# Performance work log

Hardware: AMD Instinct MI355X
Metric: run time of the kernel (lower is better)

The kernel has to match this reference:

```python
import jax, jax.numpy as jnp
import numpy as np

B, F, V = 64, 256, 128   # groups, frames/group, vecs/group (uniform ragged groups)
CF = 512                 # cross_feature


def setup_inputs() -> dict:
    key = jax.random.key(0)
    ks = jax.random.split(key, 18)
    p = lambda k, s: jax.random.normal(k, s, jnp.float32) * 0.02
    return {
        "metas": jax.random.uniform(ks[0], (B, 5), jnp.float32),
        "meta_indexs": jnp.arange(B),
        "frames": jax.random.normal(ks[1], (B * F, 600), jnp.float32),
        "frame_indexs": jnp.repeat(jnp.arange(B), F),
        "vecs": jax.random.normal(ks[2], (B * V, 768), jnp.float32),
        "vec_indexs": jnp.repeat(jnp.arange(B), V),
        "audios": jax.random.normal(ks[3], (B, 128), jnp.float32),
        "audio_indexs": jnp.arange(B),
        "Wfk": p(ks[4], (CF, 600)), "Wfv": p(ks[5], (CF, 600)),
        "Wvk": p(ks[6], (CF, 768)), "Wvv": p(ks[7], (CF, 768)),
        "Wav": p(ks[8], (CF, 128)),
        "Wff_f": p(ks[9], (2, CF, CF)),
        "Wff_v": p(ks[10], (2, CF, CF)),
        "Wff_a": p(ks[11], (2, CF, CF)),
        "Wout1": p(ks[12], (768, 3 * CF + 3)),
        "Wout2": p(ks[13], (512, 768)),
        "Wout3": p(ks[14], (64, 512)),
        "Wout4": p(ks[15], (1, 64)),
    }


def reference(metas, meta_indexs, frames, frame_indexs, vecs, vec_indexs,
              audios, audio_indexs, Wfk, Wfv, Wvk, Wvv, Wav,
              Wff_f, Wff_v, Wff_a, Wout1, Wout2, Wout3, Wout4):
    # groups are uniform: reshape ragged rows into [B, n, d] (indexes are
    # contiguous repeats per setup_inputs, so the mask-gathers become reshapes)
    b = audios.shape[0]
    fb = frames.reshape(b, -1, frames.shape[-1])   # [B,F,600]
    vb = vecs.reshape(b, -1, vecs.shape[-1])       # [B,V,768]
    relu = jax.nn.relu

    f_k = relu(jnp.einsum('bfd,cd->bfc', fb, Wfk))     # [B,F,CF]
    f_v = relu(jnp.einsum('bfd,cd->bfc', fb, Wfv))
    v_k = relu(jnp.einsum('bvd,cd->bvc', vb, Wvk))     # [B,V,CF]
    v_v = relu(jnp.einsum('bvd,cd->bvc', vb, Wvv))
    a_v = relu(audios @ Wav.T)                         # [B,CF]

    # torch: softmax(mm(k, q)) with no dim on an (N,1) tensor -> dim=1 -> ones,
    # so the initial "attended" queries are plain sums of the value projections.
    f_q_p = f_v.sum(axis=1)                            # [B,CF]
    v_q_p = v_v.sum(axis=1)
    a_q_p = a_v                                        # single audio row

    for i in range(2):
        attn_f = jax.nn.softmax(jnp.einsum('bfc,bc->bf', f_k, v_q_p) / CF, axis=1)
        f_c = jnp.einsum('bf,bfc->bc', attn_f, f_v)
        f_q_n = f_c @ Wff_f[i].T + f_q_p
        attn_v = jax.nn.softmax(jnp.einsum('bvc,bc->bv', v_k, v_q_p) / CF, axis=1)
        v_c = jnp.einsum('bv,bvc->bc', attn_v, v_v)
        v_q_n = v_c @ Wff_v[i].T + v_q_p
        # audio attention is softmax over a single element -> weight 1
        a_q_n = a_v @ Wff_a[i].T + a_q_p
        f_q_p, v_q_p, a_q_p = f_q_n, v_q_n, a_q_n      # dropout is dead code

    mean = a_q_p.mean(axis=1, keepdims=True)
    std = a_q_p.std(axis=1, keepdims=True, ddof=1)     # torch.std is unbiased
    na = (a_q_p - mean) / std

    goal = metas[:, 1:2] / 1500.0
    dura = metas[:, 3:4] - metas[:, 2:3]
    dura = jnp.where(dura > 8000.0, 100.0, dura) / 100.0
    create = metas[:, 4:5] / 5.0

    feats = jnp.concatenate([f_q_p, v_q_p, na, goal, create, dura], axis=1)  # [B,1539]
    h = relu(feats @ Wout1.T)
    h = relu(h @ Wout2.T)
    h = relu(h @ Wout3.T)
    out = jax.nn.sigmoid(h @ Wout4.T)                  # [B,1]
    return out[:, 0]
```

## Files before the change

### kernel.cpp

```cpp
#include <hip/hip_runtime.h>
#include <hip/hip_bf16.h>

typedef __attribute__((ext_vector_type(4))) float f32x4;
typedef __attribute__((ext_vector_type(8))) __bf16 bf16x8;
typedef __attribute__((ext_vector_type(8))) unsigned short us8;
typedef __attribute__((ext_vector_type(4))) unsigned int u32x4;

#define LDS_AS __attribute__((address_space(3)))
#define GLB_AS __attribute__((address_space(1)))

__device__ __forceinline__ float bf2f(unsigned short h) {
    return __builtin_bit_cast(float, (unsigned)h << 16);
}
__device__ __forceinline__ unsigned short f2bf(float f) {
    return __builtin_bit_cast(unsigned short, (__bf16)f);
}
__device__ __forceinline__ us8 cvt8(f32x4 a, f32x4 b) {
    bf16x8 r;
    r[0] = (__bf16)a[0]; r[1] = (__bf16)a[1]; r[2] = (__bf16)a[2]; r[3] = (__bf16)a[3];
    r[4] = (__bf16)b[0]; r[5] = (__bf16)b[1]; r[6] = (__bf16)b[2]; r[7] = (__bf16)b[3];
    return __builtin_bit_cast(us8, r);
}
__device__ __forceinline__ void cp16(const void* g, void* l) {
    __builtin_amdgcn_global_load_lds((const GLB_AS unsigned int*)g,
                                     (LDS_AS unsigned int*)l, 16, 0, 0);
}

#define NPREPB 2048
#define NTOT 2588672
__global__ __launch_bounds__(256) void prep_kernel(
    const float* __restrict__ frames, const float* __restrict__ Wfk, const float* __restrict__ Wfv,
    const float* __restrict__ vecs, const float* __restrict__ Wvk, const float* __restrict__ Wvv,
    const float* __restrict__ Wout1, const float* __restrict__ audios, const float* __restrict__ Wav,
    unsigned short* __restrict__ fbf, unsigned short* __restrict__ wf,
    unsigned short* __restrict__ vbf, unsigned short* __restrict__ wv,
    float* __restrict__ W1p, float* __restrict__ hacc, float* __restrict__ qz,
    float* __restrict__ a_v, float* __restrict__ a_q_p)
{
    __shared__ float aud[128];
    const int t = threadIdx.x;
    if (blockIdx.x >= NPREPB) {
        const int b = blockIdx.x - NPREPB;
        if (t < 128) aud[t] = audios[b * 128 + t];
        __syncthreads();
        #pragma unroll
        for (int cc = 0; cc < 2; ++cc) {
            int c = 2 * t + cc;
            const float* wr = Wav + (size_t)c * 128;
            float s = 0.f;
            #pragma unroll
            for (int k4 = 0; k4 < 32; ++k4) {
                f32x4 wvv = *(const f32x4*)(wr + k4 * 4);
                s += wvv[0] * aud[k4 * 4] + wvv[1] * aud[k4 * 4 + 1]
                   + wvv[2] * aud[k4 * 4 + 2] + wvv[3] * aud[k4 * 4 + 3];
            }
            s = s > 0.f ? s : 0.f;
            a_v[b * 512 + c] = s;
            a_q_p[b * 512 + c] = s;
        }
        return;
    }
    for (int i = blockIdx.x * 256 + t; i < NTOT; i += NPREPB * 256) {
        int idx = i;
        if (idx < 1245184) {
            int row = idx / 76, k = (idx - row * 76) * 8;
            us8 o = {0, 0, 0, 0, 0, 0, 0, 0};
            if (k < 600) {
                const float* s = frames + (size_t)row * 600 + k;
                o = cvt8(*(const f32x4*)s, *(const f32x4*)(s + 4));
            }
            *(us8*)(fbf + (size_t)row * 608 + k) = o;
            continue;
        }
        idx -= 1245184;
        if (idx < 77824) {
            int row = idx / 76, k = (idx - row * 76) * 8;
            const float* src = row < 512 ? Wfk + (size_t)row * 600 : Wfv + (size_t)(row - 512) * 600;
            us8 o = {0, 0, 0, 0, 0, 0, 0, 0};
            if (k < 600) o = cvt8(*(const f32x4*)(src + k), *(const f32x4*)(src + k + 4));
            *(us8*)(wf + (size_t)row * 608 + k) = o;
            continue;
        }
        idx -= 77824;
        if (idx < 786432) {
            int row = idx / 96, k = (idx - row * 96) * 8;
            const float* s = vecs + (size_t)row * 768 + k;
            *(us8*)(vbf + (size_t)row * 768 + k) = cvt8(*(const f32x4*)s, *(const f32x4*)(s + 4));
            continue;
        }
        idx -= 786432;
        if (idx < 98304) {
            int row = idx / 96, k = (idx - row * 96) * 8;
            const float* src = (row < 512 ? Wvk + (size_t)row * 768
                                          : Wvv + (size_t)(row - 512) * 768) + k;
            *(us8*)(wv + (size_t)row * 768 + k) = cvt8(*(const f32x4*)src, *(const f32x4*)(src + 4));
            continue;
        }
        idx -= 98304;
        if (idx < 344064) {
            int r = idx / 448, k = (idx - r * 448) * 4;
            f32x4 o;
            #pragma unroll
            for (int j = 0; j < 4; ++j) {
                int kk = k + j;
                o[j] = kk < 1539 ? Wout1[(size_t)r * 1539 + kk] : 0.f;
            }
            *(f32x4*)(W1p + (size_t)r * 1792 + k) = o;
            continue;
        }
        idx -= 344064;
        if (idx < 20480) {
            f32x4 z = {0, 0, 0, 0};
            *(f32x4*)(hacc + (size_t)idx * 4) = z;
            continue;
        }
        idx -= 20480;
        {
            f32x4 z = {0, 0, 0, 0};
            *(f32x4*)(qz + (size_t)idx * 4) = z;
        }
    }
}

__global__ __launch_bounds__(256) void gemm_bt_relu(
    const unsigned short* __restrict__ Af, const unsigned short* __restrict__ Bf,
    unsigned short* __restrict__ Cfo, float* __restrict__ qf,
    const unsigned short* __restrict__ Av, const unsigned short* __restrict__ Bv,
    unsigned short* __restrict__ Cvo, float* __restrict__ qv)
{
    __shared__ alignas(16) unsigned short sA[3][4096];
    __shared__ alignas(16) unsigned short sB[3][4096];
    const int t = threadIdx.x;
    const int w = t >> 6, l = t & 63;
    const unsigned short *A, *B;
    unsigned short* C;
    float* qout;
    int Kp, ktiles, gshift, nwg, pb;
    if (blockIdx.x < 1024) { A = Af; B = Bf; C = Cfo; qout = qf; Kp = 608; ktiles = 19; gshift = 8; nwg = 1024; pb = blockIdx.x; }
    else                   { A = Av; B = Bv; C = Cvo; qout = qv; Kp = 768; ktiles = 24; gshift = 7; nwg = 512;  pb = blockIdx.x - 1024; }
    const int swz = (pb & 7) * (nwg >> 3) + (pb >> 3);
    const int bm = swz >> 3, bn = swz & 7;
    const int m0 = bm << 7, n0 = bn << 7;

    const int srow = t >> 2, sk0 = (t & 3) << 3;
    const unsigned short* gA = A + (size_t)(m0 + srow) * Kp + sk0;
    const unsigned short* gB = B + (size_t)(n0 + srow) * Kp + sk0;

    const int wr = w >> 1, wc = w & 1;
    const int fAoff = (wr * 64 + (l & 15)) * 32 + ((l >> 4) << 3);
    const int fBoff = (wc * 64 + (l & 15)) * 32 + ((l >> 4) << 3);

    auto stage = [&](int buf, int kt) {
        char* lA = (char*)(&sA[buf][0]) + w * 1024;
        char* lB = (char*)(&sB[buf][0]) + w * 1024;
        const unsigned short* ga = gA + kt * 32;
        const unsigned short* gb = gB + kt * 32;
        cp16(ga, lA);
        cp16(ga + (size_t)64 * Kp, lA + 4096);
        cp16(gb, lB);
        cp16(gb + (size_t)64 * Kp, lB + 4096);
    };

    stage(0, 0);
    stage(1, 1);
    f32x4 acc[4][4] = {};
    int cur = 0;
    for (int kt = 0; kt < ktiles; ++kt) {
        if (kt + 1 < ktiles) {
            asm volatile("s_waitcnt vmcnt(4)" ::: "memory");
        } else {
            asm volatile("s_waitcnt vmcnt(0)" ::: "memory");
        }
        __builtin_amdgcn_sched_barrier(0);
        __builtin_amdgcn_s_barrier();
        __builtin_amdgcn_sched_barrier(0);

        bf16x8 af[4], bfr[4];
        #pragma unroll
        for (int i = 0; i < 4; ++i) {
            af[i]  = *(const bf16x8*)(&sA[cur][0] + fAoff + i * 512);
            bfr[i] = *(const bf16x8*)(&sB[cur][0] + fBoff + i * 512);
        }
        #pragma unroll
        for (int mi = 0; mi < 4; ++mi)
            #pragma unroll
            for (int ni = 0; ni < 4; ++ni)
                acc[mi][ni] = __builtin_amdgcn_mfma_f32_16x16x32_bf16(af[mi], bfr[ni], acc[mi][ni], 0, 0, 0);

        if (kt + 2 < ktiles) {
            int b2 = cur + 2; if (b2 >= 3) b2 -= 3;
            stage(b2, kt + 2);
        }
        cur = (cur + 1 == 3) ? 0 : cur + 1;
    }

    const int crow0 = m0 + wr * 64 + ((l >> 4) << 2);
    const int ccol0 = n0 + wc * 64 + (l & 15);
    #pragma unroll
    for (int mi = 0; mi < 4; ++mi)
        #pragma unroll
        for (int ni = 0; ni < 4; ++ni)
            #pragma unroll
            for (int j = 0; j < 4; ++j) {
                float v = acc[mi][ni][j];
                v = v > 0.f ? v : 0.f;
                C[(size_t)(crow0 + mi * 16 + j) * 1024 + (ccol0 + ni * 16)] = f2bf(v);
            }
    if (n0 >= 512) {
        const int g = m0 >> gshift;
        float csum[4];
        #pragma unroll
        for (int ni = 0; ni < 4; ++ni) {
            float s = 0.f;
            #pragma unroll
            for (int mi = 0; mi < 4; ++mi)
                #pragma unroll
                for (int j = 0; j < 4; ++j)
                    s += fmaxf(acc[mi][ni][j], 0.f);
            s += __shfl_xor(s, 16, 64);
            s += __shfl_xor(s, 32, 64);
            csum[ni] = s;
        }
        if (l < 16) {
            #pragma unroll
            for (int ni = 0; ni < 4; ++ni)
                atomicAdd(&qout[g * 512 + (ccol0 - 512) + ni * 16], csum[ni]);
        }
    }
}

__global__ __launch_bounds__(256) void scores_kernel(
    const unsigned short* __restrict__ Cf, const unsigned short* __restrict__ Cv,
    const float* __restrict__ v_q_p, float* __restrict__ sbuf, float* __restrict__ fvz)
{
    const int t = threadIdx.x, bid = blockIdx.x;
    if (bid < 64) {
        f32x4 z = {0, 0, 0, 0};
        ((f32x4*)fvz)[bid * 256 + t] = z;
    }
    const int w = t >> 6, l = t & 63;
    int fbase, g, soff;
    const unsigned short* X;
    if (bid < 1024) { fbase = bid * 16 + w * 4; g = fbase >> 8; X = Cf; soff = 0; }
    else            { fbase = (bid - 1024) * 16 + w * 4; g = fbase >> 7; X = Cv; soff = 16384; }
    const float* vq = v_q_p + g * 512 + l * 8;
    f32x4 q0 = *(const f32x4*)vq;
    f32x4 q1 = *(const f32x4*)(vq + 4);
    #pragma unroll
    for (int i = 0; i < 4; ++i) {
        const int frame = fbase + i;
        u32x4 u = *(const u32x4*)(X + (size_t)frame * 1024 + l * 8);
        float acc = q0[0] * bf2f((unsigned short)(u[0] & 0xffff)) + q0[1] * bf2f((unsigned short)(u[0] >> 16))
                  + q0[2] * bf2f((unsigned short)(u[1] & 0xffff)) + q0[3] * bf2f((unsigned short)(u[1] >> 16))
                  + q1[0] * bf2f((unsigned short)(u[2] & 0xffff)) + q1[1] * bf2f((unsigned short)(u[2] >> 16))
                  + q1[2] * bf2f((unsigned short)(u[3] & 0xffff)) + q1[3] * bf2f((unsigned short)(u[3] >> 16));
        #pragma unroll
        for (int m = 1; m < 64; m <<= 1) acc += __shfl_xor(acc, m, 64);
        if (l == 0) sbuf[soff + frame] = acc * (1.f / 512.f);
    }
}

__global__ __launch_bounds__(256) void pv_kernel(
    const unsigned short* __restrict__ Cf, const unsigned short* __restrict__ Cv,
    const float* __restrict__ sbuf, float* __restrict__ fc, float* __restrict__ vc)
{
    __shared__ float ws[256];
    __shared__ float red[256];
    const int t = threadIdx.x, bid = blockIdx.x;
    int g, chunk, NF, soff;
    const unsigned short* X;
    float* outp;
    if (bid < 1024) { g = bid >> 4; chunk = bid & 15; NF = 256; X = Cf; soff = g * 256; outp = fc; }
    else { int b2 = bid - 1024; g = b2 >> 3; chunk = b2 & 7; NF = 128; X = Cv; soff = 16384 + g * 128; outp = vc; }
    float s = (t < NF) ? sbuf[soff + t] : -1e30f;
    red[t] = s;
    __syncthreads();
    for (int st = 128; st > 0; st >>= 1) { if (t < st) red[t] = fmaxf(red[t], red[t + st]); __syncthreads(); }
    float m = red[0];
    __syncthreads();
    float e = (t < NF) ? __expf(s - m) : 0.f;
    ws[t] = e;
    red[t] = e;
    __syncthreads();
    for (int st = 128; st > 0; st >>= 1) { if (t < st) red[t] += red[t + st]; __syncthreads(); }
    float inv = 1.f / red[0];
    const int f0 = g * NF + chunk * 16;
    const unsigned int* q = (const unsigned int*)X + (size_t)f0 * 512 + 256 + t;
    float s0 = 0.f, s1 = 0.f;
    #pragma unroll 4
    for (int f = 0; f < 16; ++f) {
        float a = ws[chunk * 16 + f];
        unsigned u = q[(size_t)f * 512];
        s0 += a * bf2f((unsigned short)(u & 0xffff));
        s1 += a * bf2f((unsigned short)(u >> 16));
    }
    atomicAdd(&outp[g * 512 + 2 * t],     s0 * inv);
    atomicAdd(&outp[g * 512 + 2 * t + 1], s1 * inv);
}

__device__ __forceinline__ void gemv_body(
    const float* __restrict__ X, int ldx, int dorelu,
    const float* __restrict__ W, int ldw, float* __restrict__ Y, int ldy,
    int nc, int kc, int bc)
{
    __shared__ float xs[4096];
    const int t = threadIdx.x;
    #pragma unroll
    for (int j = 0; j < 16; ++j) {
        int idx = t + j * 256;
        float v = X[(size_t)(bc * 32 + (idx >> 7)) * ldx + kc * 128 + (idx & 127)];
        xs[idx] = dorelu ? (v > 0.f ? v : 0.f) : v;
    }
    __syncthreads();
    const int r = t & 63, bg = t >> 6;
    const int row = nc * 64 + r;
    const float* wrow = W + (size_t)row * ldw + kc * 128;
    float acc[8] = {};
    #pragma unroll 8
    for (int k4 = 0; k4 < 32; ++k4) {
        f32x4 wvv = *(const f32x4*)(wrow + k4 * 4);
        #pragma unroll
        for (int bb = 0; bb < 8; ++bb) {
            f32x4 xv = *(const f32x4*)(xs + (bg * 8 + bb) * 128 + k4 * 4);
            acc[bb] += wvv[0] * xv[0] + wvv[1] * xv[1] + wvv[2] * xv[2] + wvv[3] * xv[3];
        }
    }
    #pragma unroll
    for (int bb = 0; bb < 8; ++bb)
        atomicAdd(&Y[(size_t)(bc * 32 + bg * 8 + bb) * ldy + row], acc[bb]);
}

__global__ __launch_bounds__(256) void update_kernel(
    const float* __restrict__ Wff_f, const float* __restrict__ Wff_v, const float* __restrict__ Wff_a,
    int iter, const float* __restrict__ fc, const float* __restrict__ vc, const float* __restrict__ a_v,
    float* __restrict__ f_q_p, float* __restrict__ v_q_p, float* __restrict__ a_q_p)
{
    int id = blockIdx.x;
    const int op = id >> 6; id &= 63;
    const int nc = id & 7, kc = (id >> 3) & 3, bc = id >> 5;
    const float* W = (op == 0 ? Wff_f : op == 1 ? Wff_v : Wff_a) + (size_t)iter * 262144;
    const float* X = op == 0 ? fc : op == 1 ? vc : a_v;
    float* Y = op == 0 ? f_q_p : op == 1 ? v_q_p : a_q_p;
    gemv_body(X, 512, 0, W, 512, Y, 512, nc, kc, bc);
}

__global__ __launch_bounds__(256) void gemvb_kernel(
    const float* __restrict__ X, int ldx, int dorelu,
    const float* __restrict__ W, int ldw, float* __restrict__ Y, int ldy,
    int NC, int KC)
{
    int bid = blockIdx.x;
    const int nc = bid % NC; bid /= NC;
    const int kc = bid % KC;
    const int bc = bid / KC;
    gemv_body(X, ldx, dorelu, W, ldw, Y, ldy, nc, kc, bc);
}

__global__ __launch_bounds__(512) void normfeats_kernel(
    const float* __restrict__ a_q_p, const float* __restrict__ f_q_p, const float* __restrict__ v_q_p,
    const float* __restrict__ metas, float* __restrict__ feats)
{
    __shared__ float red[512];
    const int t = threadIdx.x, b = blockIdx.x;
    float a = a_q_p[b * 512 + t];
    red[t] = a;
    __syncthreads();
    for (int s = 256; s > 0; s >>= 1) { if (t < s) red[t] += red[t + s]; __syncthreads(); }
    float mean = red[0] * (1.f / 512.f);
    __syncthreads();
    float d = a - mean;
    red[t] = d * d;
    __syncthreads();
    for (int s = 256; s > 0; s >>= 1) { if (t < s) red[t] += red[t + s]; __syncthreads(); }
    float sd = sqrtf(red[0] * (1.f / 511.f));
    float* fr = feats + (size_t)b * 1792;
    fr[t]        = f_q_p[b * 512 + t];
    fr[512 + t]  = v_q_p[b * 512 + t];
    fr[1024 + t] = d / sd;
    if (t < 256) {
        float v = 0.f;
        if (t == 0) v = metas[b * 5 + 1] * (1.f / 1500.f);
        else if (t == 1) v = metas[b * 5 + 4] * 0.2f;
        else if (t == 2) {
            float du = metas[b * 5 + 3] - metas[b * 5 + 2];
            v = (du > 8000.f ? 100.f : du) * 0.01f;
        }
        fr[1536 + t] = v;
    }
}

__global__ __launch_bounds__(256) void mlp34_kernel(
    const float* __restrict__ h2acc, const float* __restrict__ W3, const float* __restrict__ W4,
    float* __restrict__ out)
{
    __shared__ float xs[512];
    __shared__ float part[256];
    __shared__ float h3[64];
    const int t = threadIdx.x, b = blockIdx.x;
    {
        float v0 = h2acc[(size_t)b * 512 + t];
        float v1 = h2acc[(size_t)b * 512 + 256 + t];
        xs[t] = v0 > 0.f ? v0 : 0.f;
        xs[256 + t] = v1 > 0.f ? v1 : 0.f;
    }
    __syncthreads();
    const int r = t & 63, q = t >> 6;
    const float* wrow = W3 + (size_t)r * 512 + q * 128;
    float acc = 0.f;
    #pragma unroll 8
    for (int k4 = 0; k4 < 32; ++k4) {
        f32x4 wvv = *(const f32x4*)(wrow + k4 * 4);
        f32x4 xv  = *(const f32x4*)(xs + q * 128 + k4 * 4);
        acc += wvv[0] * xv[0] + wvv[1] * xv[1] + wvv[2] * xv[2] + wvv[3] * xv[3];
    }
    part[t] = acc;
    __syncthreads();
    if (t < 64) {
        float h = part[t] + part[t + 64] + part[t + 128] + part[t + 192];
        h3[t] = h > 0.f ? h : 0.f;
    }
    __syncthreads();
    if (t < 64) {
        float v = h3[t] * W4[t];
        #pragma unroll
        for (int m = 1; m < 64; m <<= 1) v += __shfl_xor(v, m, 64);
        if (t == 0) out[b] = 1.f / (1.f + __expf(-v));
    }
}

extern "C" void kernel_launch(void* const* d_in, const int* in_sizes, int n_in,
                              void* d_out, int out_size, void* d_ws, size_t ws_size,
                              hipStream_t stream)
{
    const float* metas  = (const float*)d_in[0];
    const float* frames = (const float*)d_in[2];
    const float* vecs   = (const float*)d_in[4];
    const float* audios = (const float*)d_in[6];
    const float* Wfk   = (const float*)d_in[8];
    const float* Wfv   = (const float*)d_in[9];
    const float* Wvk   = (const float*)d_in[10];
    const float* Wvv   = (const float*)d_in[11];
    const float* Wav   = (const float*)d_in[12];
    const float* Wff_f = (const float*)d_in[13];
    const float* Wff_v = (const float*)d_in[14];
    const float* Wff_a = (const float*)d_in[15];
    const float* Wout1 = (const float*)d_in[16];
    const float* Wout2 = (const float*)d_in[17];
    const float* Wout3 = (const float*)d_in[18];
    const float* Wout4 = (const float*)d_in[19];
    float* out = (float*)d_out;

    char* p = (char*)d_ws;
    auto alloc = [&](size_t n) { char* r = p; p += (n + 255) & ~(size_t)255; return r; };
    unsigned short* fbf = (unsigned short*)alloc(16384ull * 608 * 2);
    unsigned short* wf  = (unsigned short*)alloc(1024ull * 608 * 2);
    unsigned short* vbf = (unsigned short*)alloc(8192ull * 768 * 2);
    unsigned short* wv  = (unsigned short*)alloc(1024ull * 768 * 2);
    unsigned short* Cf  = (unsigned short*)alloc(16384ull * 1024 * 2);
    unsigned short* Cv  = (unsigned short*)alloc(8192ull * 1024 * 2);
    float* W1p   = (float*)alloc(768ull * 1792 * 4);
    float* feats = (float*)alloc(64ull * 1792 * 4);
    float* qbuf  = (float*)alloc(2ull * 64 * 512 * 4);
    float* f_q_p = qbuf;
    float* v_q_p = qbuf + 64 * 512;
    float* a_q_p = (float*)alloc(64ull * 512 * 4);
    float* a_v   = (float*)alloc(64ull * 512 * 4);
    float* fvc   = (float*)alloc(2ull * 64 * 512 * 4);
    float* fcb   = fvc;
    float* vcb   = fvc + 64 * 512;
    float* hacc  = (float*)alloc(81920ull * 4);
    float* h1acc = hacc;
    float* h2acc = hacc + 64 * 768;
    float* sbuf  = (float*)alloc(24576ull * 4);

    prep_kernel<<<NPREPB + 64, 256, 0, stream>>>(frames, Wfk, Wfv, vecs, Wvk, Wvv, Wout1,
                                                 audios, Wav, fbf, wf, vbf, wv, W1p, hacc,
                                                 qbuf, a_v, a_q_p);
    gemm_bt_relu<<<1536, 256, 0, stream>>>(fbf, wf, Cf, f_q_p, vbf, wv, Cv, v_q_p);
    for (int i = 0; i < 2; ++i) {
        scores_kernel<<<1536, 256, 0, stream>>>(Cf, Cv, v_q_p, sbuf, fvc);
        pv_kernel<<<1536, 256, 0, stream>>>(Cf, Cv, sbuf, fcb, vcb);
        update_kernel<<<192, 256, 0, stream>>>(Wff_f, Wff_v, Wff_a, i, fcb, vcb, a_v,
                                               f_q_p, v_q_p, a_q_p);
    }
    normfeats_kernel<<<64, 512, 0, stream>>>(a_q_p, f_q_p, v_q_p, metas, feats);
    gemvb_kernel<<<336, 256, 0, stream>>>(feats, 1792, 0, W1p, 1792, h1acc, 768, 12, 14);
    gemvb_kernel<<<96, 256, 0, stream>>>(h1acc, 768, 1, Wout2, 768, h2acc, 512, 8, 6);
    mlp34_kernel<<<64, 256, 0, stream>>>(h2acc, Wout3, Wout4, out);
}
```

Measured before the change: 176.4 us.

## Fuse fp32-to-bf16 activation conversion into the projection GEMM A-tile load

```diff
diff --git a/kernel.cpp b/kernel.cpp
--- a/kernel.cpp
+++ b/kernel.cpp
@@ -3,6 +3,7 @@
 
 typedef __attribute__((ext_vector_type(4))) float f32x4;
 typedef __attribute__((ext_vector_type(8))) __bf16 bf16x8;
+typedef __attribute__((ext_vector_type(4))) unsigned short us4;
 typedef __attribute__((ext_vector_type(8))) unsigned short us8;
 typedef __attribute__((ext_vector_type(4))) unsigned int u32x4;
 
@@ -26,14 +27,13 @@
                                      (LDS_AS unsigned int*)l, 16, 0, 0);
 }
 
-#define NPREPB 2048
-#define NTOT 2588672
+#define NPREPB 544
+#define NTOT 557056
 __global__ __launch_bounds__(256) void prep_kernel(
-    const float* __restrict__ frames, const float* __restrict__ Wfk, const float* __restrict__ Wfv,
-    const float* __restrict__ vecs, const float* __restrict__ Wvk, const float* __restrict__ Wvv,
+    const float* __restrict__ Wfk, const float* __restrict__ Wfv,
+    const float* __restrict__ Wvk, const float* __restrict__ Wvv,
     const float* __restrict__ Wout1, const float* __restrict__ audios, const float* __restrict__ Wav,
-    unsigned short* __restrict__ fbf, unsigned short* __restrict__ wf,
-    unsigned short* __restrict__ vbf, unsigned short* __restrict__ wv,
+    unsigned short* __restrict__ wf, unsigned short* __restrict__ wv,
     float* __restrict__ W1p, float* __restrict__ hacc, float* __restrict__ qz,
     float* __restrict__ a_v, float* __restrict__ a_q_p)
 {
@@ -62,17 +62,6 @@
     }
     for (int i = blockIdx.x * 256 + t; i < NTOT; i += NPREPB * 256) {
         int idx = i;
-        if (idx < 1245184) {
-            int row = idx / 76, k = (idx - row * 76) * 8;
-            us8 o = {0, 0, 0, 0, 0, 0, 0, 0};
-            if (k < 600) {
-                const float* s = frames + (size_t)row * 600 + k;
-                o = cvt8(*(const f32x4*)s, *(const f32x4*)(s + 4));
-            }
-            *(us8*)(fbf + (size_t)row * 608 + k) = o;
-            continue;
-        }
-        idx -= 1245184;
         if (idx < 77824) {
             int row = idx / 76, k = (idx - row * 76) * 8;
             const float* src = row < 512 ? Wfk + (size_t)row * 600 : Wfv + (size_t)(row - 512) * 600;
@@ -82,13 +71,6 @@
             continue;
         }
         idx -= 77824;
-        if (idx < 786432) {
-            int row = idx / 96, k = (idx - row * 96) * 8;
-            const float* s = vecs + (size_t)row * 768 + k;
-            *(us8*)(vbf + (size_t)row * 768 + k) = cvt8(*(const f32x4*)s, *(const f32x4*)(s + 4));
-            continue;
-        }
-        idx -= 786432;
         if (idx < 98304) {
             int row = idx / 96, k = (idx - row * 96) * 8;
             const float* src = (row < 512 ? Wvk + (size_t)row * 768
@@ -122,58 +104,78 @@
     }
 }
 
-__global__ __launch_bounds__(256) void gemm_bt_relu(
-    const unsigned short* __restrict__ Af, const unsigned short* __restrict__ Bf,
+__global__ __launch_bounds__(256) void gemm_fused(
+    const float* __restrict__ Aff, const unsigned short* __restrict__ Bf,
     unsigned short* __restrict__ Cfo, float* __restrict__ qf,
-    const unsigned short* __restrict__ Av, const unsigned short* __restrict__ Bv,
+    const float* __restrict__ Afv, const unsigned short* __restrict__ Bv,
     unsigned short* __restrict__ Cvo, float* __restrict__ qv)
 {
     __shared__ alignas(16) unsigned short sA[3][4096];
     __shared__ alignas(16) unsigned short sB[3][4096];
     const int t = threadIdx.x;
     const int w = t >> 6, l = t & 63;
-    const unsigned short *A, *B;
+    const float* A;
+    const unsigned short* B;
     unsigned short* C;
     float* qout;
-    int Kp, ktiles, gshift, nwg, pb;
-    if (blockIdx.x < 1024) { A = Af; B = Bf; C = Cfo; qout = qf; Kp = 608; ktiles = 19; gshift = 8; nwg = 1024; pb = blockIdx.x; }
-    else                   { A = Av; B = Bv; C = Cvo; qout = qv; Kp = 768; ktiles = 24; gshift = 7; nwg = 512;  pb = blockIdx.x - 1024; }
+    int Kreal, Kp, ktiles, gshift, nwg, pb;
+    if (blockIdx.x < 1024) { A = Aff; B = Bf; C = Cfo; qout = qf; Kreal = 600; Kp = 608; ktiles = 19; gshift = 8; nwg = 1024; pb = blockIdx.x; }
+    else                   { A = Afv; B = Bv; C = Cvo; qout = qv; Kreal = 768; Kp = 768; ktiles = 24; gshift = 7; nwg = 512;  pb = blockIdx.x - 1024; }
     const int swz = (pb & 7) * (nwg >> 3) + (pb >> 3);
     const int bm = swz >> 3, bn = swz & 7;
     const int m0 = bm << 7, n0 = bn << 7;
 
     const int srow = t >> 2, sk0 = (t & 3) << 3;
-    const unsigned short* gA = A + (size_t)(m0 + srow) * Kp + sk0;
     const unsigned short* gB = B + (size_t)(n0 + srow) * Kp + sk0;
+    const int arow = w * 32 + (l >> 3);
+    const int acol = (l & 7) * 4;
+    const float* gA = A + (size_t)(m0 + arow) * Kreal + acol;
+    const int wAidx = arow * 32 + acol;
 
     const int wr = w >> 1, wc = w & 1;
     const int fAoff = (wr * 64 + (l & 15)) * 32 + ((l >> 4) << 3);
     const int fBoff = (wc * 64 + (l & 15)) * 32 + ((l >> 4) << 3);
 
-    auto stage = [&](int buf, int kt) {
-        char* lA = (char*)(&sA[buf][0]) + w * 1024;
+    f32x4 av[4];
+    auto loadA = [&](int kt) {
+        const bool ok = (kt * 32 + acol) < Kreal;
+        const float* ga = gA + kt * 32;
+        #pragma unroll
+        for (int j = 0; j < 4; ++j)
+            av[j] = ok ? *(const f32x4*)(ga + (size_t)j * 8 * Kreal)
+                       : f32x4{0.f, 0.f, 0.f, 0.f};
+    };
+    auto writeA = [&](int buf) {
+        unsigned short* wA = &sA[buf][0] + wAidx;
+        #pragma unroll
+        for (int j = 0; j < 4; ++j) {
+            us4 o = {f2bf(av[j][0]), f2bf(av[j][1]), f2bf(av[j][2]), f2bf(av[j][3])};
+            *(us4*)(wA + j * 256) = o;
+        }
+    };
+    auto stageB = [&](int buf, int kt) {
         char* lB = (char*)(&sB[buf][0]) + w * 1024;
-        const unsigned short* ga = gA + kt * 32;
         const unsigned short* gb = gB + kt * 32;
-        cp16(ga, lA);
-        cp16(ga + (size_t)64 * Kp, lA + 4096);
         cp16(gb, lB);
         cp16(gb + (size_t)64 * Kp, lB + 4096);
     };
 
-    stage(0, 0);
-    stage(1, 1);
+    loadA(0);
+    stageB(0, 0);
+    stageB(1, 1);
+    asm volatile("s_waitcnt vmcnt(4)" ::: "memory");
+    writeA(0);
+    asm volatile("s_waitcnt vmcnt(2)" ::: "memory");
+    asm volatile("s_waitcnt lgkmcnt(0)" ::: "memory");
+    __builtin_amdgcn_s_barrier();
+
     f32x4 acc[4][4] = {};
     int cur = 0;
     for (int kt = 0; kt < ktiles; ++kt) {
-        if (kt + 1 < ktiles) {
-            asm volatile("s_waitcnt vmcnt(4)" ::: "memory");
-        } else {
-            asm volatile("s_waitcnt vmcnt(0)" ::: "memory");
-        }
-        __builtin_amdgcn_sched_barrier(0);
-        __builtin_amdgcn_s_barrier();
-        __builtin_amdgcn_sched_barrier(0);
+        int nxt = cur + 1; if (nxt == 3) nxt = 0;
+        int nx2 = nxt + 1; if (nx2 == 3) nx2 = 0;
+        if (kt + 1 < ktiles) loadA(kt + 1);
+        if (kt + 2 < ktiles) stageB(nx2, kt + 2);
 
         bf16x8 af[4], bfr[4];
         #pragma unroll
@@ -187,11 +189,17 @@
             for (int ni = 0; ni < 4; ++ni)
                 acc[mi][ni] = __builtin_amdgcn_mfma_f32_16x16x32_bf16(af[mi], bfr[ni], acc[mi][ni], 0, 0, 0);
 
-        if (kt + 2 < ktiles) {
-            int b2 = cur + 2; if (b2 >= 3) b2 -= 3;
-            stage(b2, kt + 2);
-        }
-        cur = (cur + 1 == 3) ? 0 : cur + 1;
+        if (kt + 1 < ktiles) {
+            if (kt + 2 < ktiles) asm volatile("s_waitcnt vmcnt(2)" ::: "memory");
+            else                 asm volatile("s_waitcnt vmcnt(0)" ::: "memory");
+            __builtin_amdgcn_sched_barrier(0);
+            writeA(nxt);
+            asm volatile("s_waitcnt lgkmcnt(0)" ::: "memory");
+            __builtin_amdgcn_sched_barrier(0);
+            __builtin_amdgcn_s_barrier();
+            __builtin_amdgcn_sched_barrier(0);
+        }
+        cur = nxt;
     }
 
     const int crow0 = m0 + wr * 64 + ((l >> 4) << 2);
@@ -452,9 +460,7 @@
 
     char* p = (char*)d_ws;
     auto alloc = [&](size_t n) { char* r = p; p += (n + 255) & ~(size_t)255; return r; };
-    unsigned short* fbf = (unsigned short*)alloc(16384ull * 608 * 2);
     unsigned short* wf  = (unsigned short*)alloc(1024ull * 608 * 2);
-    unsigned short* vbf = (unsigned short*)alloc(8192ull * 768 * 2);
     unsigned short* wv  = (unsigned short*)alloc(1024ull * 768 * 2);
     unsigned short* Cf  = (unsigned short*)alloc(16384ull * 1024 * 2);
     unsigned short* Cv  = (unsigned short*)alloc(8192ull * 1024 * 2);
@@ -473,10 +479,9 @@
     float* h2acc = hacc + 64 * 768;
     float* sbuf  = (float*)alloc(24576ull * 4);
 
-    prep_kernel<<<NPREPB + 64, 256, 0, stream>>>(frames, Wfk, Wfv, vecs, Wvk, Wvv, Wout1,
-                                                 audios, Wav, fbf, wf, vbf, wv, W1p, hacc,
-                                                 qbuf, a_v, a_q_p);
-    gemm_bt_relu<<<1536, 256, 0, stream>>>(fbf, wf, Cf, f_q_p, vbf, wv, Cv, v_q_p);
+    prep_kernel<<<NPREPB + 64, 256, 0, stream>>>(Wfk, Wfv, Wvk, Wvv, Wout1, audios, Wav,
+                                                 wf, wv, W1p, hacc, qbuf, a_v, a_q_p);
+    gemm_fused<<<1536, 256, 0, stream>>>(frames, wf, Cf, f_q_p, vecs, wv, Cv, v_q_p);
     for (int i = 0; i < 2; ++i) {
         scores_kernel<<<1536, 256, 0, stream>>>(Cf, Cv, v_q_p, sbuf, fvc);
         pv_kernel<<<1536, 256, 0, stream>>>(Cf, Cv, sbuf, fcb, vcb);
```

Result: slower. 181.0 us (+2.6%).
